# Kernel tuning notes

Hardware: AMD Instinct MI355X
Metric: run time of the kernel (lower is better)

Reference implementation:

```python
import jax, jax.numpy as jnp
import numpy as np

N_NODES = 20000
N_EDGES = 320000
IN_CH = 512
HID = 128
HEADS = 4
OUT_CH = 30
NEG_SLOPE = 0.2  # PyG GATConv default negative_slope


def add_self_loops(ei, n):
    loops = jnp.arange(n, dtype=ei.dtype)
    return jnp.concatenate([ei, jnp.stack([loops, loops])], axis=1)


def gat_layer(x, ei, W, a_src, a_dst, b, concat):
    # x: [N, F_in], ei: [2, E] (source row 0 -> target row 1), W: [F_in, H*C]
    n = x.shape[0]
    H, C = a_src.shape
    h = (x @ W).reshape(n, H, C)                      # [N, H, C]
    src, dst = ei[0], ei[1]
    al_src = jnp.einsum('nhc,hc->nh', h, a_src)       # [N, H]
    al_dst = jnp.einsum('nhc,hc->nh', h, a_dst)
    e = al_src[src] + al_dst[dst]                     # [E, H]
    e = jnp.where(e > 0, e, NEG_SLOPE * e)            # LeakyReLU
    # segment softmax over destination nodes (stable)
    emax = jax.lax.stop_gradient(jax.ops.segment_max(e, dst, num_segments=n))
    p = jnp.exp(e - emax[dst])
    denom = jax.ops.segment_sum(p, dst, num_segments=n)
    alpha = p / denom[dst]                            # [E, H]
    msg = h[src] * alpha[:, :, None]                  # [E, H, C]
    out = jax.ops.segment_sum(msg, dst, num_segments=n)  # [N, H, C]
    out = out.reshape(n, H * C) if concat else out.mean(axis=1)
    return out + b


def setup_inputs() -> dict:
    key = jax.random.key(0)
    ks = jax.random.split(key, 12)
    s = 0.05
    x = jax.random.normal(ks[0], (N_NODES, IN_CH), jnp.float32)
    edge_index = jax.random.randint(ks[1], (2, N_EDGES), 0, N_NODES, jnp.int32)
    return {
        'x': x,
        'edge_index': edge_index,
        'W1': jax.random.normal(ks[2], (IN_CH, HEADS * HID), jnp.float32) * s,
        'a_src1': jax.random.normal(ks[3], (HEADS, HID), jnp.float32) * s,
        'a_dst1': jax.random.normal(ks[4], (HEADS, HID), jnp.float32) * s,
        'b1': jnp.zeros((HEADS * HID,), jnp.float32),
        'W2': jax.random.normal(ks[5], (HEADS * HID, OUT_CH), jnp.float32) * s,
        'a_src2': jax.random.normal(ks[6], (1, OUT_CH), jnp.float32) * s,
        'a_dst2': jax.random.normal(ks[7], (1, OUT_CH), jnp.float32) * s,
        'b2': jnp.zeros((OUT_CH,), jnp.float32),
        'Wd': jax.random.normal(ks[8], (OUT_CH, IN_CH), jnp.float32) * s,
        'bd': jnp.zeros((IN_CH,), jnp.float32),
    }


def reference(x, edge_index, W1, a_src1, a_dst1, b1, W2, a_src2, a_dst2, b2, Wd, bd):
    n = x.shape[0]
    ei = add_self_loops(edge_index, n)
    h = gat_layer(x, ei, W1, a_src1, a_dst1, b1, concat=True)   # [N, HEADS*HID]
    h = jax.nn.elu(h)                                           # dropout is identity in eval
    z = gat_layer(h, ei, W2, a_src2, a_dst2, b2, concat=False)  # [N, OUT_CH]
    x_hat = z @ Wd + bd                                         # [N, IN_CH]
    return (x_hat, z)
```

## Files before the change

kernel.cpp:

```cpp
#include <hip/hip_runtime.h>
#include <hip/hip_bf16.h>
#include <stdint.h>

#define N_NODES 20000
#define N_EDGES 320000
#define IN_CH 512
#define HID 128
#define HEADS 4
#define HC 512
#define OUT_CH 30
#define NEG_SLOPE 0.2f
#define M_PAD 20096
#define PARTS 79
#define CAST_BLOCKS (M_PAD * IN_CH / 4 / 256)
#define G1_BLOCKS (M_PAD / 64 * 4)
#define CNT_BLOCKS (N_EDGES / 256)

typedef _Float16 half8 __attribute__((ext_vector_type(8)));
typedef _Float16 half4v __attribute__((ext_vector_type(4)));
typedef float f32x4 __attribute__((ext_vector_type(4)));

static __device__ __forceinline__ float lrelu(float e) { return e > 0.f ? e : NEG_SLOPE * e; }

static __device__ __forceinline__ void gload16(const void* gsrc, void* ldst) {
  __builtin_amdgcn_global_load_lds(
      (const __attribute__((address_space(1))) uint32_t*)gsrc,
      (__attribute__((address_space(3))) uint32_t*)ldst,
      16, 0, 0);
}

__global__ __launch_bounds__(256) void k_front(const float* __restrict__ x,
                                               const float* __restrict__ W1,
                                               const float* __restrict__ W2,
                                               _Float16* __restrict__ xh,
                                               _Float16* __restrict__ W1t,
                                               _Float16* __restrict__ w2t,
                                               int* __restrict__ cnt) {
  __shared__ float t[64][65];
  const int b = blockIdx.x;
  const int tid = threadIdx.x;
  if (b < CAST_BLOCKS) {
    int i = b * 256 + tid;
    if (i < N_NODES) cnt[i] = 0;
    int base = i * 4;
    int row = base >> 9;
    half4v o;
    if (row < N_NODES) {
      float4 v = *(const float4*)(x + (size_t)base);
      o[0] = (_Float16)v.x; o[1] = (_Float16)v.y; o[2] = (_Float16)v.z; o[3] = (_Float16)v.w;
    } else {
      o[0] = o[1] = o[2] = o[3] = (_Float16)0.f;
    }
    *(half4v*)(xh + (size_t)base) = o;
  } else if (b < CAST_BLOCKS + 64) {
    const int bb = b - CAST_BLOCKS;
    const int bk = (bb & 7) * 64;
    const int bn = (bb >> 3) * 64;
#pragma unroll
    for (int it = 0; it < 16; it++) {
      int idx = tid + it * 256;
      int r = idx >> 6, c = idx & 63;
      t[r][c] = W1[(size_t)(bk + r) * HC + bn + c];
    }
    __syncthreads();
#pragma unroll
    for (int it = 0; it < 16; it++) {
      int idx = tid + it * 256;
      int rn = idx >> 6, ck = idx & 63;
      W1t[(size_t)(bn + rn) * IN_CH + bk + ck] = (_Float16)t[ck][rn];
    }
  } else {
    int idx = (b - CAST_BLOCKS - 64) * 256 + tid;
    int n = idx >> 9, k = idx & 511;
    w2t[idx] = (n < OUT_CH) ? (_Float16)W2[(size_t)k * OUT_CH + n] : (_Float16)0.f;
  }
}

__global__ __launch_bounds__(256) void k_gemm1_mfma(const _Float16* __restrict__ A,
                                                    const _Float16* __restrict__ Bt,
                                                    _Float16* __restrict__ C,
                                                    const float* __restrict__ a_src,
                                                    const float* __restrict__ a_dst,
                                                    float* __restrict__ al_s,
                                                    float* __restrict__ al_d,
                                                    const int* __restrict__ dst,
                                                    int* __restrict__ cnt) {
  __shared__ _Float16 smem[64 * 64 + 128 * 64];
  const int bx = blockIdx.x;
  const int tid = threadIdx.x;
  if (bx >= G1_BLOCKS) {
    int e = (bx - G1_BLOCKS) * 256 + tid;
    atomicAdd(&cnt[dst[e]], 1);
    return;
  }
  _Float16* As = smem;
  _Float16* Bs = smem + 64 * 64;
  _Float16* Cs = smem;
  const int lane = tid & 63;
  const int w = tid >> 6;
  const int bm = (bx >> 2) * 64;
  const int head = bx & 3;
  const int bn = head * 128;

  const int lrow = lane >> 3;
  const int schunk = (lane & 7) ^ lrow;
  const int r15 = lane & 15;
  const int q = lane >> 4;

  f32x4 acc[8];
  const f32x4 zero = {0.f, 0.f, 0.f, 0.f};
#pragma unroll
  for (int j = 0; j < 8; j++) acc[j] = zero;

  for (int kb = 0; kb < 8; kb++) {
    const int kof = kb * 64 + schunk * 8;
#pragma unroll
    for (int t = 0; t < 2; t++) {
      const int row = w * 16 + t * 8;
      gload16(A + (size_t)(bm + row + lrow) * IN_CH + kof, (void*)(As + row * 64));
    }
#pragma unroll
    for (int t = 0; t < 4; t++) {
      const int row = w * 32 + t * 8;
      gload16(Bt + (size_t)(bn + row + lrow) * IN_CH + kof, (void*)(Bs + row * 64));
    }
    __syncthreads();
#pragma unroll
    for (int s = 0; s < 2; s++) {
      const int cs = ((s * 4 + q) ^ (lane & 7)) * 8;
      half8 af = *(const half8*)&As[(w * 16 + r15) * 64 + cs];
#pragma unroll
      for (int j = 0; j < 8; j++) {
        half8 bf = *(const half8*)&Bs[(j * 16 + r15) * 64 + cs];
        acc[j] = __builtin_amdgcn_mfma_f32_16x16x32_f16(af, bf, acc[j], 0, 0, 0);
      }
    }
    __syncthreads();
  }
#pragma unroll
  for (int j = 0; j < 8; j++)
#pragma unroll
    for (int r = 0; r < 4; r++) {
      const int row = w * 16 + q * 4 + r;
      const int col = j * 16 + r15;
      Cs[row * 136 + col] = (_Float16)acc[j][r];
    }
  __syncthreads();
#pragma unroll
  for (int it = 0; it < 4; it++) {
    int cidx = tid + it * 256;
    int row = cidx >> 4, c16 = cidx & 15;
    int gm = bm + row;
    if (gm < N_NODES)
      *(half8*)(C + (size_t)gm * HC + bn + c16 * 8) = *(const half8*)&Cs[row * 136 + c16 * 8];
  }
  const int row = tid >> 2;
  const int qr = tid & 3;
  const float* asp = a_src + head * HID + qr * 32;
  const float* adp = a_dst + head * HID + qr * 32;
  float s = 0.f, d = 0.f;
#pragma unroll
  for (int j8 = 0; j8 < 4; j8++) {
    half8 cv = *(const half8*)&Cs[row * 136 + qr * 32 + j8 * 8];
    float4 a0 = *(const float4*)(asp + j8 * 8);
    float4 a1 = *(const float4*)(asp + j8 * 8 + 4);
    float4 d0 = *(const float4*)(adp + j8 * 8);
    float4 d1 = *(const float4*)(adp + j8 * 8 + 4);
    float c0 = (float)cv[0], c1 = (float)cv[1], c2 = (float)cv[2], c3 = (float)cv[3];
    float c4 = (float)cv[4], c5 = (float)cv[5], c6 = (float)cv[6], c7 = (float)cv[7];
    s += c0 * a0.x + c1 * a0.y + c2 * a0.z + c3 * a0.w +
         c4 * a1.x + c5 * a1.y + c6 * a1.z + c7 * a1.w;
    d += c0 * d0.x + c1 * d0.y + c2 * d0.z + c3 * d0.w +
         c4 * d1.x + c5 * d1.y + c6 * d1.z + c7 * d1.w;
  }
  s += __shfl_xor(s, 1);
  s += __shfl_xor(s, 2);
  d += __shfl_xor(d, 1);
  d += __shfl_xor(d, 2);
  const int gm = bm + row;
  if (qr == 0 && gm < N_NODES) {
    al_s[gm * HEADS + head] = s;
    al_d[gm * HEADS + head] = d;
  }
}

__global__ __launch_bounds__(256) void k_scan_part(const int* __restrict__ cnt,
                                                   int* __restrict__ part) {
  __shared__ int ws[4];
  int i = blockIdx.x * 256 + threadIdx.x;
  int v = (i < N_NODES) ? cnt[i] : 0;
  int lane = threadIdx.x & 63;
#pragma unroll
  for (int off = 32; off; off >>= 1) v += __shfl_down(v, off);
  if (lane == 0) ws[threadIdx.x >> 6] = v;
  __syncthreads();
  if (threadIdx.x == 0) part[blockIdx.x] = ws[0] + ws[1] + ws[2] + ws[3];
}
__global__ __launch_bounds__(256) void k_scan_final(const int* __restrict__ cnt,
                                                    const int* __restrict__ part,
                                                    int* __restrict__ offs,
                                                    int* __restrict__ cursor) {
  __shared__ int buf[256];
  __shared__ int s_prefix;
  const int b = blockIdx.x;
  const int t = threadIdx.x;
  if (t < 64) {
    int v = 0;
    for (int j = t; j < b; j += 64) v += part[j];
#pragma unroll
    for (int off = 32; off; off >>= 1) v += __shfl_down(v, off);
    if (t == 0) s_prefix = v;
  }
  int i = b * 256 + t;
  int v = (i < N_NODES) ? cnt[i] : 0;
  buf[t] = v;
  __syncthreads();
#pragma unroll
  for (int off = 1; off < 256; off <<= 1) {
    int x = (t >= off) ? buf[t - off] : 0;
    __syncthreads();
    buf[t] += x;
    __syncthreads();
  }
  if (i < N_NODES) {
    int ex = s_prefix + buf[t] - v;
    offs[i] = ex;
    cursor[i] = ex;
  }
  if (b == PARTS - 1 && t == 255) offs[N_NODES] = s_prefix + buf[255];
}
__global__ void k_scatter(const int* __restrict__ src, const int* __restrict__ dst,
                          int* __restrict__ cursor, int* __restrict__ srcs) {
  int e = blockIdx.x * blockDim.x + threadIdx.x;
  if (e < N_EDGES) {
    int pos = atomicAdd(&cursor[dst[e]], 1);
    srcs[pos] = src[e];
  }
}

__global__ __launch_bounds__(256) void k_agg1(const _Float16* __restrict__ h,
                                              const float* __restrict__ al_s,
                                              const float* __restrict__ al_d,
                                              const int* __restrict__ offs,
                                              const int* __restrict__ srcs,
                                              const float* __restrict__ b1,
                                              _Float16* __restrict__ hm) {
  __shared__ __align__(16) int2 s_sp[4][64];
  const int tid = threadIdx.x;
  const int lane = tid & 63;
  const int wv = tid >> 6;
  const int qq = lane >> 4;
  const int l16 = lane & 15;
  const int head = blockIdx.x / 1250;
  const int n = (blockIdx.x % 1250) * 16 + wv * 4 + qq;
  const int cb = head * HID + l16 * 8;

  const float adn = al_d[n * HEADS + head];
  const float pself = __expf(lrelu(al_s[n * HEADS + head] + adn));

  half8 hv = *(const half8*)(h + (size_t)n * HC + cb);
  float acc[8];
  float den = pself;
#pragma unroll
  for (int j = 0; j < 8; j++) acc[j] = pself * (float)hv[j];

  const int beg = offs[n];
  const int cnt = offs[n + 1] - beg;
  int mx = cnt;
  mx = max(mx, __shfl_xor(mx, 16));
  mx = max(mx, __shfl_xor(mx, 32));

  for (int base = 0; base < mx; base += 16) {
    int sreg = n;
    float preg = 0.f;
    if (base + l16 < cnt) {
      sreg = srcs[beg + base + l16];
      preg = __expf(lrelu(al_s[sreg * HEADS + head] + adn));
    }
    s_sp[wv][lane] = make_int2(sreg, __float_as_int(preg));
    __builtin_amdgcn_wave_barrier();
    const int rem = cnt - base;
    const int m4 = rem > 16 ? 16 : ((rem + 3) & ~3);
    for (int k = 0; k < m4; k += 4) {
      int4 w0 = *(const int4*)&s_sp[wv][qq * 16 + k];
      int4 w1 = *(const int4*)&s_sp[wv][qq * 16 + k + 2];
      half8 v0 = *(const half8*)(h + (size_t)w0.x * HC + cb);
      half8 v1 = *(const half8*)(h + (size_t)w0.z * HC + cb);
      half8 v2 = *(const half8*)(h + (size_t)w1.x * HC + cb);
      half8 v3 = *(const half8*)(h + (size_t)w1.z * HC + cb);
      float p0 = __int_as_float(w0.y), p1 = __int_as_float(w0.w);
      float p2 = __int_as_float(w1.y), p3 = __int_as_float(w1.w);
      den += p0 + p1 + p2 + p3;
#pragma unroll
      for (int j = 0; j < 8; j++)
        acc[j] += p0 * (float)v0[j] + p1 * (float)v1[j] +
                  p2 * (float)v2[j] + p3 * (float)v3[j];
    }
    __builtin_amdgcn_wave_barrier();
  }
  const float inv = 1.f / den;
  float4 bb0 = *(const float4*)(b1 + cb);
  float4 bb1 = *(const float4*)(b1 + cb + 4);
  float ob[8] = {bb0.x, bb0.y, bb0.z, bb0.w, bb1.x, bb1.y, bb1.z, bb1.w};
  half8 ov;
#pragma unroll
  for (int j = 0; j < 8; j++) {
    float o = acc[j] * inv + ob[j];
    o = o > 0.f ? o : __expf(o) - 1.f;
    ov[j] = (_Float16)o;
  }
  *(half8*)(hm + (size_t)n * HC + cb) = ov;
}

__global__ __launch_bounds__(256) void k_gemm2_mfma(const _Float16* __restrict__ hm,
                                                    const _Float16* __restrict__ w2t,
                                                    const float* __restrict__ a_s2,
                                                    const float* __restrict__ a_d2,
                                                    float* __restrict__ zpre,
                                                    float* __restrict__ al_s2,
                                                    float* __restrict__ al_d2) {
  __shared__ _Float16 Bs[32 * 520];
  __shared__ _Float16 As[64 * 136];
  const int tid = threadIdx.x;
  const int lane = tid & 63;
  const int w = tid >> 6;
  const int bm = blockIdx.x * 64;
  const int n15 = lane & 15;
  const int q = lane >> 4;

#pragma unroll
  for (int it = 0; it < 8; it++) {
    int idx = (tid + it * 256) * 8;
    int n = idx >> 9, k = idx & 511;
    *(half8*)&Bs[n * 520 + k] = *(const half8*)(w2t + idx);
  }

  f32x4 acc0 = {0.f, 0.f, 0.f, 0.f}, acc1 = {0.f, 0.f, 0.f, 0.f};
  for (int kt = 0; kt < HC; kt += 128) {
#pragma unroll
    for (int p = 0; p < 4; p++) {
      int row = (tid >> 4) + p * 16;
      int kof = (tid & 15) * 8;
      int gm = bm + row;
      half8 v = {};
      if (gm < N_NODES) v = *(const half8*)(hm + (size_t)gm * HC + kt + kof);
      *(half8*)&As[row * 136 + kof] = v;
    }
    __syncthreads();
#pragma unroll
    for (int ks = 0; ks < 128; ks += 32) {
      half8 af = *(const half8*)&As[(w * 16 + n15) * 136 + ks + q * 8];
      half8 b0 = *(const half8*)&Bs[n15 * 520 + kt + ks + q * 8];
      half8 b1 = *(const half8*)&Bs[(16 + n15) * 520 + kt + ks + q * 8];
      acc0 = __builtin_amdgcn_mfma_f32_16x16x32_f16(af, b0, acc0, 0, 0, 0);
      acc1 = __builtin_amdgcn_mfma_f32_16x16x32_f16(af, b1, acc1, 0, 0, 0);
    }
    __syncthreads();
  }
  const float asn0 = (n15 < OUT_CH) ? a_s2[n15] : 0.f;
  const float asn1 = (n15 + 16 < OUT_CH) ? a_s2[n15 + 16] : 0.f;
  const float adn0 = (n15 < OUT_CH) ? a_d2[n15] : 0.f;
  const float adn1 = (n15 + 16 < OUT_CH) ? a_d2[n15 + 16] : 0.f;
#pragma unroll
  for (int r = 0; r < 4; r++) {
    const int gm = bm + w * 16 + q * 4 + r;
    const bool ok = gm < N_NODES;
    if (ok) {
      zpre[(size_t)gm * OUT_CH + n15] = acc0[r];
      if (n15 + 16 < OUT_CH) zpre[(size_t)gm * OUT_CH + n15 + 16] = acc1[r];
    }
    float s = acc0[r] * asn0 + acc1[r] * asn1;
    float d = acc0[r] * adn0 + acc1[r] * adn1;
#pragma unroll
    for (int off = 8; off; off >>= 1) {
      s += __shfl_xor(s, off);
      d += __shfl_xor(d, off);
    }
    if (n15 == 0 && ok) {
      al_s2[gm] = s;
      al_d2[gm] = d;
    }
  }
}

__global__ __launch_bounds__(256) void k_agg2(const float* __restrict__ zpre,
                                              const float* __restrict__ al_s2,
                                              const float* __restrict__ al_d2,
                                              const int* __restrict__ offs,
                                              const int* __restrict__ srcs,
                                              const float* __restrict__ b2,
                                              float* __restrict__ zout) {
  __shared__ __align__(16) int2 s_sp[4][64];
  const int tid = threadIdx.x;
  const int lane = tid & 63;
  const int wv = tid >> 6;
  const int hh = lane >> 5;
  const int l32 = lane & 31;
  const int n = blockIdx.x * 8 + wv * 2 + hh;
  const float ad2n = al_d2[n];
  const float pself = __expf(lrelu(al_s2[n] + ad2n));
  const bool act = l32 < OUT_CH;
  float zv = act ? zpre[(size_t)n * OUT_CH + l32] : 0.f;
  float acc = pself * zv;
  float den = pself;

  const int beg = offs[n];
  const int cnt = offs[n + 1] - beg;
  int mx = max(cnt, __shfl_xor(cnt, 32));

  for (int base = 0; base < mx; base += 32) {
    int sreg = n;
    float preg = 0.f;
    if (base + l32 < cnt) {
      sreg = srcs[beg + base + l32];
      preg = __expf(lrelu(al_s2[sreg] + ad2n));
    }
    s_sp[wv][lane] = make_int2(sreg, __float_as_int(preg));
    __builtin_amdgcn_wave_barrier();
    const int rem = cnt - base;
    const int m4 = rem > 32 ? 32 : ((rem + 3) & ~3);
    for (int k = 0; k < m4; k += 4) {
      int4 w0 = *(const int4*)&s_sp[wv][hh * 32 + k];
      int4 w1 = *(const int4*)&s_sp[wv][hh * 32 + k + 2];
      float v0 = act ? zpre[(size_t)w0.x * OUT_CH + l32] : 0.f;
      float v1 = act ? zpre[(size_t)w0.z * OUT_CH + l32] : 0.f;
      float v2 = act ? zpre[(size_t)w1.x * OUT_CH + l32] : 0.f;
      float v3 = act ? zpre[(size_t)w1.z * OUT_CH + l32] : 0.f;
      float p0 = __int_as_float(w0.y), p1 = __int_as_float(w0.w);
      float p2 = __int_as_float(w1.y), p3 = __int_as_float(w1.w);
      den += p0 + p1 + p2 + p3;
      acc += p0 * v0 + p1 * v1 + p2 * v2 + p3 * v3;
    }
    __builtin_amdgcn_wave_barrier();
  }
  if (act) zout[(size_t)n * OUT_CH + l32] = acc / den + b2[l32];
}

__global__ __launch_bounds__(256) void k_dec(const float* __restrict__ z,
                                             const float* __restrict__ Wd,
                                             const float* __restrict__ bd,
                                             float* __restrict__ xhat) {
  __shared__ float zs[64][32];
  const int tid = threadIdx.x;
  const int c = blockIdx.y * 256 + tid;
  float wd[32];
#pragma unroll
  for (int k = 0; k < OUT_CH; k++) wd[k] = Wd[(size_t)k * IN_CH + c];
  wd[30] = wd[31] = 0.f;
  const int n0 = blockIdx.x * 64;
  for (int idx = tid; idx < 64 * 32; idx += 256) {
    int r = idx >> 5, cc = idx & 31;
    int row = n0 + r;
    zs[r][cc] = (cc < OUT_CH && row < N_NODES) ? z[(size_t)row * OUT_CH + cc] : 0.f;
  }
  __syncthreads();
  const float b0 = bd[c];
  for (int i = 0; i < 64; i++) {
    int row = n0 + i;
    if (row >= N_NODES) break;
    float a0 = b0;
#pragma unroll
    for (int k4 = 0; k4 < 8; k4++) {
      float4 zv = *(const float4*)&zs[i][k4 * 4];
      a0 += zv.x * wd[k4 * 4 + 0] + zv.y * wd[k4 * 4 + 1] +
            zv.z * wd[k4 * 4 + 2] + zv.w * wd[k4 * 4 + 3];
    }
    xhat[(size_t)row * IN_CH + c] = a0;
  }
}

extern "C" void kernel_launch(void* const* d_in, const int* in_sizes, int n_in,
                              void* d_out, int out_size, void* d_ws, size_t ws_size,
                              hipStream_t stream) {
  const float* x    = (const float*)d_in[0];
  const int*   ei   = (const int*)d_in[1];
  const float* W1   = (const float*)d_in[2];
  const float* a_s1 = (const float*)d_in[3];
  const float* a_d1 = (const float*)d_in[4];
  const float* b1   = (const float*)d_in[5];
  const float* W2   = (const float*)d_in[6];
  const float* a_s2 = (const float*)d_in[7];
  const float* a_d2 = (const float*)d_in[8];
  const float* b2   = (const float*)d_in[9];
  const float* Wd   = (const float*)d_in[10];
  const float* bd   = (const float*)d_in[11];

  float* xhat = (float*)d_out;
  float* zout = xhat + (size_t)N_NODES * IN_CH;

  const int* srcv = ei;
  const int* dstv = ei + N_EDGES;

  char* w = (char*)d_ws;
  auto alloc = [&](size_t bytes) {
    void* p = (void*)w;
    w += (bytes + 255) & ~(size_t)255;
    return p;
  };
  _Float16* xh   = (_Float16*)alloc((size_t)M_PAD * IN_CH * 2);
  _Float16* w1t  = (_Float16*)alloc((size_t)HC * IN_CH * 2);
  _Float16* w2t  = (_Float16*)alloc((size_t)32 * HC * 2);
  _Float16* h    = (_Float16*)alloc((size_t)N_NODES * HC * 2);
  _Float16* hm   = (_Float16*)alloc((size_t)N_NODES * HC * 2);
  float* zpre  = (float*)alloc((size_t)N_NODES * OUT_CH * 4);
  float* al_s1v= (float*)alloc((size_t)N_NODES * HEADS * 4);
  float* al_d1v= (float*)alloc((size_t)N_NODES * HEADS * 4);
  float* al_s2v= (float*)alloc((size_t)N_NODES * 4);
  float* al_d2v= (float*)alloc((size_t)N_NODES * 4);
  int*   cnt   = (int*)alloc((size_t)N_NODES * 4);
  int*   offs  = (int*)alloc((size_t)(N_NODES + 1) * 4);
  int*   cursor= (int*)alloc((size_t)N_NODES * 4);
  int*   srcs  = (int*)alloc((size_t)N_EDGES * 4);
  int*   part  = (int*)alloc((size_t)PARTS * 4);

  const int EB = (N_EDGES + 255) / 256;

  k_front<<<CAST_BLOCKS + 128, 256, 0, stream>>>(x, W1, W2, xh, w1t, w2t, cnt);
  k_gemm1_mfma<<<G1_BLOCKS + CNT_BLOCKS, 256, 0, stream>>>(xh, w1t, h, a_s1, a_d1,
                                                           al_s1v, al_d1v, dstv, cnt);
  k_scan_part<<<PARTS, 256, 0, stream>>>(cnt, part);
  k_scan_final<<<PARTS, 256, 0, stream>>>(cnt, part, offs, cursor);
  k_scatter<<<EB, 256, 0, stream>>>(srcv, dstv, cursor, srcs);
  k_agg1<<<1250 * HEADS, 256, 0, stream>>>(h, al_s1v, al_d1v, offs, srcs, b1, hm);
  k_gemm2_mfma<<<(N_NODES + 63) / 64, 256, 0, stream>>>(hm, w2t, a_s2, a_d2, zpre,
                                                        al_s2v, al_d2v);
  k_agg2<<<N_NODES / 8, 256, 0, stream>>>(zpre, al_s2v, al_d2v, offs, srcs, b2, zout);
  k_dec<<<dim3((N_NODES + 63) / 64, 2), 256, 0, stream>>>(zout, Wd, bd, xhat);
}
```

Before: 259.8 us.

## Fuse fp32-to-fp16 input cast into GEMM1 A-tile load and interleave edge counting

Removes the separate pass that converted x to an fp16 staging buffer. GEMM1 now reads fp32 x directly, converts it in registers and writes swizzled fp16 tiles to LDS, with row bounds checks replacing the zero padding. Edge-count atomic blocks are interleaved with GEMM blocks in the grid so both kinds of work share the device. This saves a full write and re-read of the staging buffer, but the A path loses async global-to-LDS loads and each tile now costs more register work and twice the fp32 bytes, read once per head (four times).

```diff
diff --git a/kernel.cpp b/kernel.cpp
--- a/kernel.cpp
+++ b/kernel.cpp
@@ -12,7 +12,6 @@
 #define NEG_SLOPE 0.2f
 #define M_PAD 20096
 #define PARTS 79
-#define CAST_BLOCKS (M_PAD * IN_CH / 4 / 256)
 #define G1_BLOCKS (M_PAD / 64 * 4)
 #define CNT_BLOCKS (N_EDGES / 256)
 
@@ -29,33 +28,17 @@
       16, 0, 0);
 }
 
-__global__ __launch_bounds__(256) void k_front(const float* __restrict__ x,
-                                               const float* __restrict__ W1,
+__global__ __launch_bounds__(256) void k_front(const float* __restrict__ W1,
                                                const float* __restrict__ W2,
-                                               _Float16* __restrict__ xh,
                                                _Float16* __restrict__ W1t,
                                                _Float16* __restrict__ w2t,
                                                int* __restrict__ cnt) {
   __shared__ float t[64][65];
   const int b = blockIdx.x;
   const int tid = threadIdx.x;
-  if (b < CAST_BLOCKS) {
-    int i = b * 256 + tid;
-    if (i < N_NODES) cnt[i] = 0;
-    int base = i * 4;
-    int row = base >> 9;
-    half4v o;
-    if (row < N_NODES) {
-      float4 v = *(const float4*)(x + (size_t)base);
-      o[0] = (_Float16)v.x; o[1] = (_Float16)v.y; o[2] = (_Float16)v.z; o[3] = (_Float16)v.w;
-    } else {
-      o[0] = o[1] = o[2] = o[3] = (_Float16)0.f;
-    }
-    *(half4v*)(xh + (size_t)base) = o;
-  } else if (b < CAST_BLOCKS + 64) {
-    const int bb = b - CAST_BLOCKS;
-    const int bk = (bb & 7) * 64;
-    const int bn = (bb >> 3) * 64;
+  if (b < 64) {
+    const int bk = (b & 7) * 64;
+    const int bn = (b >> 3) * 64;
 #pragma unroll
     for (int it = 0; it < 16; it++) {
       int idx = tid + it * 256;
@@ -69,14 +52,17 @@
       int rn = idx >> 6, ck = idx & 63;
       W1t[(size_t)(bn + rn) * IN_CH + bk + ck] = (_Float16)t[ck][rn];
     }
-  } else {
-    int idx = (b - CAST_BLOCKS - 64) * 256 + tid;
+  } else if (b < 128) {
+    int idx = (b - 64) * 256 + tid;
     int n = idx >> 9, k = idx & 511;
     w2t[idx] = (n < OUT_CH) ? (_Float16)W2[(size_t)k * OUT_CH + n] : (_Float16)0.f;
-  }
-}
-
-__global__ __launch_bounds__(256) void k_gemm1_mfma(const _Float16* __restrict__ A,
+  } else {
+    int i = (b - 128) * 256 + tid;
+    if (i < N_NODES) cnt[i] = 0;
+  }
+}
+
+__global__ __launch_bounds__(256) void k_gemm1_mfma(const float* __restrict__ X,
                                                     const _Float16* __restrict__ Bt,
                                                     _Float16* __restrict__ C,
                                                     const float* __restrict__ a_src,
@@ -88,18 +74,24 @@
   __shared__ _Float16 smem[64 * 64 + 128 * 64];
   const int bx = blockIdx.x;
   const int tid = threadIdx.x;
-  if (bx >= G1_BLOCKS) {
-    int e = (bx - G1_BLOCKS) * 256 + tid;
-    atomicAdd(&cnt[dst[e]], 1);
-    return;
+  int gx;
+  if (bx < 2 * CNT_BLOCKS) {
+    if ((bx & 1) == 0) {
+      int e = (bx >> 1) * 256 + tid;
+      atomicAdd(&cnt[dst[e]], 1);
+      return;
+    }
+    gx = bx >> 1;
+  } else {
+    gx = CNT_BLOCKS + (bx - 2 * CNT_BLOCKS);
   }
   _Float16* As = smem;
   _Float16* Bs = smem + 64 * 64;
   _Float16* Cs = smem;
   const int lane = tid & 63;
   const int w = tid >> 6;
-  const int bm = (bx >> 2) * 64;
-  const int head = bx & 3;
+  const int bm = (gx >> 2) * 64;
+  const int head = gx & 3;
   const int bn = head * 128;
 
   const int lrow = lane >> 3;
@@ -113,16 +105,30 @@
   for (int j = 0; j < 8; j++) acc[j] = zero;
 
   for (int kb = 0; kb < 8; kb++) {
-    const int kof = kb * 64 + schunk * 8;
+    const int kof = kb * 64;
 #pragma unroll
     for (int t = 0; t < 2; t++) {
-      const int row = w * 16 + t * 8;
-      gload16(A + (size_t)(bm + row + lrow) * IN_CH + kof, (void*)(As + row * 64));
+      int idx = tid + t * 256;
+      int row = idx >> 3, g = idx & 7;
+      int gm = bm + row;
+      float4 v0 = {0.f, 0.f, 0.f, 0.f}, v1 = {0.f, 0.f, 0.f, 0.f};
+      if (gm < N_NODES) {
+        const float* src = X + (size_t)gm * IN_CH + kof + g * 8;
+        v0 = *(const float4*)src;
+        v1 = *(const float4*)(src + 4);
+      }
+      half8 hv;
+      hv[0] = (_Float16)v0.x; hv[1] = (_Float16)v0.y;
+      hv[2] = (_Float16)v0.z; hv[3] = (_Float16)v0.w;
+      hv[4] = (_Float16)v1.x; hv[5] = (_Float16)v1.y;
+      hv[6] = (_Float16)v1.z; hv[7] = (_Float16)v1.w;
+      *(half8*)&As[row * 64 + ((g ^ (row & 7)) * 8)] = hv;
     }
 #pragma unroll
     for (int t = 0; t < 4; t++) {
       const int row = w * 32 + t * 8;
-      gload16(Bt + (size_t)(bn + row + lrow) * IN_CH + kof, (void*)(Bs + row * 64));
+      gload16(Bt + (size_t)(bn + row + lrow) * IN_CH + kof + schunk * 8,
+              (void*)(Bs + row * 64));
     }
     __syncthreads();
 #pragma unroll
@@ -497,7 +503,6 @@
     w += (bytes + 255) & ~(size_t)255;
     return p;
   };
-  _Float16* xh   = (_Float16*)alloc((size_t)M_PAD * IN_CH * 2);
   _Float16* w1t  = (_Float16*)alloc((size_t)HC * IN_CH * 2);
   _Float16* w2t  = (_Float16*)alloc((size_t)32 * HC * 2);
   _Float16* h    = (_Float16*)alloc((size_t)N_NODES * HC * 2);
@@ -515,8 +520,8 @@
 
   const int EB = (N_EDGES + 255) / 256;
 
-  k_front<<<CAST_BLOCKS + 128, 256, 0, stream>>>(x, W1, W2, xh, w1t, w2t, cnt);
-  k_gemm1_mfma<<<G1_BLOCKS + CNT_BLOCKS, 256, 0, stream>>>(xh, w1t, h, a_s1, a_d1,
+  k_front<<<128 + PARTS, 256, 0, stream>>>(W1, W2, w1t, w2t, cnt);
+  k_gemm1_mfma<<<G1_BLOCKS + CNT_BLOCKS, 256, 0, stream>>>(x, w1t, h, a_s1, a_d1,
                                                            al_s1v, al_d1v, dstv, cnt);
   k_scan_part<<<PARTS, 256, 0, stream>>>(cnt, part);
   k_scan_final<<<PARTS, 256, 0, stream>>>(cnt, part, offs, cursor);
```

Result: slower. 289.7 us (+11.5%).
